# Kernel tuning notes

Measured on AMD Instinct MI355X. Metric: run time of the kernel, lower is better.

Reference implementation:

```python
import jax, jax.numpy as jnp
import numpy as np
import math

IN_CH = 256
CH = 128
SCALE = math.sqrt(CH)
TEMPERATURE = 1.0


def setup_inputs() -> dict:
    key = jax.random.key(0)
    ks = jax.random.split(key, 9)
    B, C, H, W = 8, IN_CH, 56, 56
    x = jax.random.normal(ks[0], (B, C, H, W), dtype=jnp.float32)
    s_in = 1.0 / math.sqrt(IN_CH)
    s_ch = 1.0 / math.sqrt(CH)
    wq = jax.random.uniform(ks[1], (CH, IN_CH), minval=-s_in, maxval=s_in)
    bq = jax.random.uniform(ks[2], (CH,), minval=-s_in, maxval=s_in)
    wk = jax.random.uniform(ks[3], (CH, IN_CH), minval=-s_in, maxval=s_in)
    bk = jax.random.uniform(ks[4], (CH,), minval=-s_in, maxval=s_in)
    wv = jax.random.uniform(ks[5], (CH, IN_CH), minval=-s_in, maxval=s_in)
    bv = jax.random.uniform(ks[6], (CH,), minval=-s_in, maxval=s_in)
    wo = jax.random.uniform(ks[7], (IN_CH, CH), minval=-s_ch, maxval=s_ch)
    bo = jax.random.uniform(ks[8], (IN_CH,), minval=-s_ch, maxval=s_ch)
    return {"x": x, "wq": wq, "bq": bq, "wk": wk, "bk": bk,
            "wv": wv, "bv": bv, "wo": wo, "bo": bo}


def reference(x, wq, bq, wk, bk, wv, bv, wo, bo):
    B, C, H, W = x.shape
    N = H * W
    xf = x.reshape(B, C, N)  # flatten spatial; 1x1 conv == channel matmul
    q = jnp.einsum('oc,bcn->bon', wq, xf) + bq[None, :, None]  # (B,CH,N)
    k = jnp.einsum('oc,bcn->bon', wk, xf) + bk[None, :, None]
    v = jnp.einsum('oc,bcn->bon', wv, xf) + bv[None, :, None]
    # similarity map (B, N, N): query positions x key positions
    sim = jnp.einsum('bcn,bcm->bnm', q, k) / (SCALE * TEMPERATURE)
    attn = jax.nn.softmax(sim, axis=2)
    out = jnp.einsum('bnm,bcm->bnc', attn, v)  # (B, N, CH)
    out = jnp.einsum('oc,bnc->bon', wo, out) + bo[None, :, None]  # (B,IN_CH,N)
    return x + out.reshape(B, C, H, W)
```

## Files before the change

### kernel.cpp

```cpp
#include <hip/hip_runtime.h>
#include <hip/hip_bf16.h>
#include <math.h>

#define NPOS 3136
#define NB   8
#define LOG2E 1.44269504088896f
#define QSCALE (0.08838834764831845f * LOG2E)

typedef __attribute__((ext_vector_type(8))) short shortx8;
typedef __attribute__((ext_vector_type(4))) short shortx4;
typedef __attribute__((ext_vector_type(4))) float f32x4;
typedef __attribute__((ext_vector_type(16))) float f32x16;
typedef __attribute__((ext_vector_type(4))) unsigned int uint4v;

struct S8pair { shortx4 lo, hi; };

__device__ __forceinline__ float bf2f(unsigned short u) {
    unsigned int i = ((unsigned int)u) << 16;
    return __builtin_bit_cast(float, i);
}
__device__ __forceinline__ unsigned short f2bf(float f) {
    unsigned int i = __builtin_bit_cast(unsigned int, f);
    i += 0x7FFFu + ((i >> 16) & 1u);
    return (unsigned short)(i >> 16);
}
__device__ __forceinline__ void gll16(const unsigned short* g, unsigned short* l) {
    __builtin_amdgcn_global_load_lds((const __attribute__((address_space(1))) void*)g,
                                     (__attribute__((address_space(3))) void*)l, 16, 0, 0);
}

__global__ __launch_bounds__(256) void cast_w(
    const float* __restrict__ wq, const float* __restrict__ wk,
    const float* __restrict__ wv, const float* __restrict__ wo,
    unsigned short* __restrict__ Wb)
{
    const int sel = blockIdx.y;
    const float* src = (sel == 0) ? wq : (sel == 1) ? wk : (sel == 2) ? wv : wo;
    const float sc = (sel == 0) ? QSCALE : 1.0f;
    unsigned short* dst = Wb + sel * 32768;
    int i0 = (blockIdx.x * 256 + threadIdx.x) * 8;
    #pragma unroll
    for (int e = 0; e < 8; ++e) dst[i0 + e] = f2bf(src[i0 + e] * sc);
}

__global__ __launch_bounds__(256) void cast_xT(
    const float* __restrict__ x, unsigned short* __restrict__ xT)
{
    const int b = blockIdx.z, c0 = blockIdx.y * 64, n0 = blockIdx.x * 64;
    __shared__ unsigned short Ls[64 * 66];
    const int t = threadIdx.x;
    {
        int r = t >> 2, q4 = t & 3;
        const float* src = x + ((size_t)b * 256 + c0 + r) * NPOS + n0 + q4 * 16;
        #pragma unroll
        for (int i = 0; i < 16; ++i) Ls[r * 66 + q4 * 16 + i] = f2bf(src[i]);
    }
    __syncthreads();
    {
        int j = t >> 2, h4 = t & 3;
        shortx8 v0, v1;
        #pragma unroll
        for (int i = 0; i < 8; ++i) v0[i] = (short)Ls[(h4 * 16 + i) * 66 + j];
        #pragma unroll
        for (int i = 0; i < 8; ++i) v1[i] = (short)Ls[(h4 * 16 + 8 + i) * 66 + j];
        unsigned short* dst = xT + ((size_t)b * NPOS + n0 + j) * 256 + c0 + h4 * 16;
        *reinterpret_cast<shortx8*>(dst) = v0;
        *reinterpret_cast<shortx8*>(dst + 8) = v1;
    }
}

__global__ __launch_bounds__(256) void qkv_mfma(
    const unsigned short* __restrict__ xT,
    const unsigned short* __restrict__ Wb,
    const float* __restrict__ bq, const float* __restrict__ bk, const float* __restrict__ bv,
    unsigned short* __restrict__ qT, unsigned short* __restrict__ kT,
    unsigned short* __restrict__ vC)
{
    const int b = blockIdx.z, sel = blockIdx.y, n0 = blockIdx.x * 64;
    const int t = threadIdx.x, lane = t & 63, wave = t >> 6;
    const int l16 = lane & 15, lhi = lane >> 4;
    __shared__ __align__(16) unsigned short Wt[128 * 128];
    __shared__ __align__(16) unsigned short Xt[64 * 128];
    const unsigned short* Wsel = Wb + sel * 32768;
    const float* bias = (sel == 0) ? bq : (sel == 1) ? bk : bv;

    f32x4 acc[2][4];
    #pragma unroll
    for (int ab = 0; ab < 2; ++ab)
        #pragma unroll
        for (int nb = 0; nb < 4; ++nb) acc[ab][nb] = f32x4{0.f, 0.f, 0.f, 0.f};

    for (int ks0 = 0; ks0 < 2; ++ks0) {
        const int k0 = ks0 * 128;
        __syncthreads();
        #pragma unroll
        for (int i = 0; i < 8; ++i) {
            int c = (wave * 8 + i) * 64 + lane;
            int row = c >> 4, cin = (c & 15) ^ (row & 7);
            gll16(Wsel + (size_t)row * 256 + k0 + cin * 8, &Wt[0] + (wave * 8 + i) * 512);
        }
        #pragma unroll
        for (int i = 0; i < 4; ++i) {
            int c = (wave * 4 + i) * 64 + lane;
            int row = c >> 4, cin = (c & 15) ^ (row & 7);
            gll16(xT + ((size_t)b * NPOS + n0 + row) * 256 + k0 + cin * 8,
                  &Xt[0] + (wave * 4 + i) * 512);
        }
        __syncthreads();
        #pragma unroll
        for (int ks = 0; ks < 4; ++ks) {
            shortx8 aW[2];
            #pragma unroll
            for (int ab = 0; ab < 2; ++ab) {
                int row = wave * 32 + ab * 16 + l16;
                int idx = (row * 128 + ks * 32 + lhi * 8) ^ ((row & 7) << 3);
                aW[ab] = *reinterpret_cast<const shortx8*>(Wt + idx);
            }
            #pragma unroll
            for (int nb = 0; nb < 4; ++nb) {
                int row = nb * 16 + l16;
                int idx = (row * 128 + ks * 32 + lhi * 8) ^ ((row & 7) << 3);
                shortx8 bX = *reinterpret_cast<const shortx8*>(Xt + idx);
                acc[0][nb] = __builtin_amdgcn_mfma_f32_16x16x32_bf16(aW[0], bX, acc[0][nb], 0, 0, 0);
                acc[1][nb] = __builtin_amdgcn_mfma_f32_16x16x32_bf16(aW[1], bX, acc[1][nb], 0, 0, 0);
            }
        }
    }
    const int strip = wave * 32;
    if (sel < 2) {
        unsigned short* dst0 = ((sel == 0) ? qT : kT) + (size_t)b * NPOS * 128;
        const float bsc = (sel == 0) ? QSCALE : 1.0f;
        #pragma unroll
        for (int ab = 0; ab < 2; ++ab) {
            int ocb = strip + ab * 16 + lhi * 4;
            float bb[4];
            #pragma unroll
            for (int j = 0; j < 4; ++j) bb[j] = bias[ocb + j] * bsc;
            #pragma unroll
            for (int nb = 0; nb < 4; ++nb) {
                int n = n0 + nb * 16 + l16;
                shortx4 u;
                #pragma unroll
                for (int j = 0; j < 4; ++j) u[j] = (short)f2bf(acc[ab][nb][j] + bb[j]);
                *reinterpret_cast<shortx4*>(dst0 + (size_t)n * 128 + ocb) = u;
            }
        }
    } else {
        #pragma unroll
        for (int ab = 0; ab < 2; ++ab)
            #pragma unroll
            for (int j = 0; j < 4; ++j) {
                int oc = strip + ab * 16 + lhi * 4 + j;
                float bb = bias[oc];
                unsigned short* dst = vC + ((size_t)b * 128 + oc) * NPOS + n0;
                #pragma unroll
                for (int nb = 0; nb < 4; ++nb)
                    dst[nb * 16 + l16] = f2bf(acc[ab][nb][j] + bb);
            }
    }
}

__global__ __launch_bounds__(256) void attn_kernel(
    const unsigned short* __restrict__ qT,
    const unsigned short* __restrict__ kT,
    const unsigned short* __restrict__ vC,
    unsigned short* __restrict__ ao,
    float* __restrict__ lrG)
{
    const int i_lin = blockIdx.y * 49 + blockIdx.x;
    const int b = i_lin & 7;
    const int n0 = (i_lin >> 3) * 64;
    const int t = threadIdx.x, lane = t & 63, wave = t >> 6;
    const int l31 = lane & 31, h = lane >> 5;
    const int qsub = wave >> 1, kh = wave & 1;
    const int NT = NPOS / 64;

    __shared__ __align__(16) unsigned short KsB[2][64 * 128];
    __shared__ __align__(16) unsigned short VsB[2][128 * 64];

    shortx8 aQ[8];
    {
        const unsigned short* qp = qT + ((size_t)b * NPOS + n0 + qsub * 32 + l31) * 128 + h * 8;
        #pragma unroll
        for (int kk = 0; kk < 8; ++kk)
            aQ[kk] = *reinterpret_cast<const shortx8*>(qp + kk * 16);
    }

    const unsigned short* kSrc[4];
    const unsigned short* vSrc[4];
    unsigned sDst[4];
    #pragma unroll
    for (int i = 0; i < 4; ++i) {
        int c = (wave * 4 + i) * 64 + lane;
        int rK = c >> 4, cK = (c & 15) ^ (rK & 15);
        kSrc[i] = kT + ((size_t)b * NPOS + rK) * 128 + cK * 8;
        int rV = c >> 3, cV = (c & 7) ^ (rV & 7);
        vSrc[i] = vC + ((size_t)b * 128 + rV) * NPOS + cV * 8;
        sDst[i] = (wave * 4 + i) * 512;
    }

    unsigned kIdx[8];
    {
        int rowK = kh * 32 + l31;
        #pragma unroll
        for (int kk = 0; kk < 8; ++kk)
            kIdx[kk] = rowK * 128 + (((kk * 2 + h) ^ (rowK & 15)) * 8);
    }
    unsigned vIdx[4][2][2];
    #pragma unroll
    for (int ob = 0; ob < 4; ++ob) {
        int rowV = ob * 32 + l31;
        #pragma unroll
        for (int ks = 0; ks < 2; ++ks)
            #pragma unroll
            for (int rr = 0; rr < 2; ++rr)
                vIdx[ob][ks][rr] = rowV * 64 + h * 4
                    + (((kh * 4 + ks * 2 + rr) * 8) ^ ((rowV & 7) * 8));
    }

    f32x16 o[4];
    #pragma unroll
    for (int ob = 0; ob < 4; ++ob)
        #pragma unroll
        for (int r2 = 0; r2 < 16; ++r2) o[ob][r2] = 0.f;
    float lrP = 0.f;

    f32x16 FZ;
    #pragma unroll
    for (int r2 = 0; r2 < 16; ++r2) FZ[r2] = 0.f;
    asm volatile("" : "+v"(FZ));

    #define STAGE(kt_, buf_)                                                          \
        _Pragma("unroll")                                                             \
        for (int i = 0; i < 4; ++i) {                                                 \
            gll16(kSrc[i] + (size_t)(kt_) * 8192, &KsB[buf_][0] + sDst[i]);           \
            gll16(vSrc[i] + (kt_) * 64, &VsB[buf_][0] + sDst[i]);                     \
        }

    #define COMPUTE(Ks, Vs)                                                           \
    {                                                                                 \
        f32x16 s_;                                                                    \
        __builtin_amdgcn_s_setprio(1);                                                \
        {                                                                             \
            shortx8 k0 = *reinterpret_cast<const shortx8*>((Ks) + kIdx[0]);           \
            s_ = __builtin_amdgcn_mfma_f32_32x32x16_bf16(k0, aQ[0], FZ, 0, 0, 0);     \
        }                                                                             \
        _Pragma("unroll")                                                             \
        for (int kk = 1; kk < 8; ++kk) {                                              \
            shortx8 kf = *reinterpret_cast<const shortx8*>((Ks) + kIdx[kk]);          \
            s_ = __builtin_amdgcn_mfma_f32_32x32x16_bf16(kf, aQ[kk], s_, 0, 0, 0);    \
        }                                                                             \
        __builtin_amdgcn_s_setprio(0);                                                \
        unsigned pk[8];                                                               \
        _Pragma("unroll")                                                             \
        for (int g = 0; g < 4; ++g) {                                                 \
            float p0 = exp2f(s_[g * 4 + 0]);                                          \
            float p1 = exp2f(s_[g * 4 + 1]);                                          \
            float p2 = exp2f(s_[g * 4 + 2]);                                          \
            float p3 = exp2f(s_[g * 4 + 3]);                                          \
            lrP += (p0 + p1) + (p2 + p3);                                             \
            asm("v_cvt_pk_bf16_f32 %0, %1, %2" : "=v"(pk[g * 2 + 0]) : "v"(p0), "v"(p1)); \
            asm("v_cvt_pk_bf16_f32 %0, %1, %2" : "=v"(pk[g * 2 + 1]) : "v"(p2), "v"(p3)); \
        }                                                                             \
        __builtin_amdgcn_s_setprio(1);                                                \
        _Pragma("unroll")                                                             \
        for (int ks = 0; ks < 2; ++ks) {                                              \
            uint4v pv = {pk[ks * 4 + 0], pk[ks * 4 + 1], pk[ks * 4 + 2], pk[ks * 4 + 3]}; \
            shortx8 PA = __builtin_bit_cast(shortx8, pv);                             \
            _Pragma("unroll")                                                         \
            for (int ob = 0; ob < 4; ++ob) {                                          \
                shortx4 lo = *reinterpret_cast<const shortx4*>((Vs) + vIdx[ob][ks][0]); \
                shortx4 hi = *reinterpret_cast<const shortx4*>((Vs) + vIdx[ob][ks][1]); \
                shortx8 bV = __builtin_bit_cast(shortx8, S8pair{lo, hi});             \
                o[ob] = __builtin_amdgcn_mfma_f32_32x32x16_bf16(PA, bV, o[ob], 0, 0, 0); \
            }                                                                         \
        }                                                                             \
        __builtin_amdgcn_s_setprio(0);                                                \
    }

    STAGE(0, 0)
    STAGE(1, 1)

    int cur = 0;
    for (int kt = 0; kt < NT - 1; ++kt) {
        asm volatile("s_waitcnt vmcnt(8)" ::: "memory");
        __builtin_amdgcn_sched_barrier(0);
        __builtin_amdgcn_s_barrier();
        __builtin_amdgcn_sched_barrier(0);
        COMPUTE(&KsB[cur][0], &VsB[cur][0])
        __builtin_amdgcn_sched_barrier(0);
        __builtin_amdgcn_s_barrier();
        __builtin_amdgcn_sched_barrier(0);
        if (kt < NT - 2) { STAGE(kt + 2, cur) }
        cur ^= 1;
    }
    {
        asm volatile("s_waitcnt vmcnt(0)" ::: "memory");
        __builtin_amdgcn_sched_barrier(0);
        __builtin_amdgcn_s_barrier();
        COMPUTE(&KsB[cur][0], &VsB[cur][0])
    }
    __syncthreads();

    float lr2 = lrP + __shfl_xor(lrP, 32);
    float* Om = reinterpret_cast<float*>(&KsB[0][0]);
    float* lrS = reinterpret_cast<float*>(&VsB[1][0]);
    unsigned short* Oo = &VsB[0][0];

    if (kh == 1) {
        #pragma unroll
        for (int ob = 0; ob < 4; ++ob)
            #pragma unroll
            for (int r2 = 0; r2 < 16; ++r2) {
                int q = qsub * 32 + (r2 & 3) + 8 * (r2 >> 2) + 4 * h;
                Om[q * 128 + ob * 32 + l31] = o[ob][r2];
            }
        if (lane < 32) lrS[qsub * 32 + l31] = lr2;
    }
    __syncthreads();
    if (kh == 0) {
        #pragma unroll
        for (int ob = 0; ob < 4; ++ob)
            #pragma unroll
            for (int r2 = 0; r2 < 16; ++r2) {
                int q = qsub * 32 + (r2 & 3) + 8 * (r2 >> 2) + 4 * h;
                int idx = q * 128 + ob * 32 + l31;
                Oo[idx] = f2bf(o[ob][r2] + Om[idx]);
            }
        if (lane < 32)
            lrG[(size_t)b * NPOS + n0 + qsub * 32 + l31] = lr2 + lrS[qsub * 32 + l31];
    }
    __syncthreads();
    {
        const shortx8* src = reinterpret_cast<const shortx8*>(Oo);
        shortx8* dst = reinterpret_cast<shortx8*>(ao + ((size_t)b * NPOS + n0) * 128);
        #pragma unroll
        for (int i = 0; i < 4; ++i) dst[t + 256 * i] = src[t + 256 * i];
    }
    #undef STAGE
    #undef COMPUTE
}

__global__ __launch_bounds__(256) void out_proj(
    const float* __restrict__ x,
    const unsigned short* __restrict__ Wb,
    const float* __restrict__ bo,
    const unsigned short* __restrict__ ao,
    const float* __restrict__ lrG,
    float* __restrict__ y)
{
    const int b = blockIdx.y, n0 = blockIdx.x * 64;
    const int t = threadIdx.x, lane = t & 63, wave = t >> 6;
    const int l16 = lane & 15, lhi = lane >> 4;
    __shared__ __align__(16) unsigned short Wt[256 * 128];
    __shared__ __align__(16) unsigned short At[64 * 128];
    const unsigned short* wo = Wb + 98304;

    #pragma unroll
    for (int i = 0; i < 16; ++i) {
        int c = (wave * 16 + i) * 64 + lane;
        int row = c >> 4, cin = (c & 15) ^ (row & 7);
        gll16(wo + (size_t)row * 128 + cin * 8, &Wt[0] + (wave * 16 + i) * 512);
    }
    #pragma unroll
    for (int i = 0; i < 4; ++i) {
        int c = (wave * 4 + i) * 64 + lane;
        int row = c >> 4, cin = (c & 15) ^ (row & 7);
        gll16(ao + ((size_t)b * NPOS + n0 + row) * 128 + cin * 8, &At[0] + (wave * 4 + i) * 512);
    }
    __syncthreads();

    f32x4 acc[4][4];
    #pragma unroll
    for (int ab = 0; ab < 4; ++ab)
        #pragma unroll
        for (int nb = 0; nb < 4; ++nb) acc[ab][nb] = f32x4{0.f, 0.f, 0.f, 0.f};

    const int strip = wave * 64;
    #pragma unroll
    for (int ks = 0; ks < 4; ++ks) {
        shortx8 aW[4];
        #pragma unroll
        for (int ab = 0; ab < 4; ++ab) {
            int row = strip + ab * 16 + l16;
            int idx = (row * 128 + ks * 32 + lhi * 8) ^ ((row & 7) << 3);
            aW[ab] = *reinterpret_cast<const shortx8*>(Wt + idx);
        }
        #pragma unroll
        for (int nb = 0; nb < 4; ++nb) {
            int row = nb * 16 + l16;
            int idx = (row * 128 + ks * 32 + lhi * 8) ^ ((row & 7) << 3);
            shortx8 bA = *reinterpret_cast<const shortx8*>(At + idx);
            #pragma unroll
            for (int ab = 0; ab < 4; ++ab)
                acc[ab][nb] = __builtin_amdgcn_mfma_f32_16x16x32_bf16(aW[ab], bA, acc[ab][nb], 0, 0, 0);
        }
    }

    float inv[4];
    #pragma unroll
    for (int nb = 0; nb < 4; ++nb)
        inv[nb] = 1.0f / lrG[(size_t)b * NPOS + n0 + nb * 16 + l16];

    #pragma unroll
    for (int ab = 0; ab < 4; ++ab)
        #pragma unroll
        for (int j = 0; j < 4; ++j) {
            int oc = strip + ab * 16 + lhi * 4 + j;
            float bb = bo[oc];
            const float* xr = x + ((size_t)b * 256 + oc) * NPOS + n0;
            float* yr = y + ((size_t)b * 256 + oc) * NPOS + n0;
            #pragma unroll
            for (int nb = 0; nb < 4; ++nb) {
                int n = nb * 16 + l16;
                yr[n] = xr[n] + bb + acc[ab][nb][j] * inv[nb];
            }
        }
}

extern "C" void kernel_launch(void* const* d_in, const int* in_sizes, int n_in,
                              void* d_out, int out_size, void* d_ws, size_t ws_size,
                              hipStream_t stream)
{
    const float* x  = (const float*)d_in[0];
    const float* wq = (const float*)d_in[1];
    const float* bq = (const float*)d_in[2];
    const float* wk = (const float*)d_in[3];
    const float* bk = (const float*)d_in[4];
    const float* wv = (const float*)d_in[5];
    const float* bv = (const float*)d_in[6];
    const float* wo = (const float*)d_in[7];
    const float* bo = (const float*)d_in[8];
    float* y = (float*)d_out;

    const size_t sz = (size_t)NB * NPOS * 128;
    unsigned short* qT = (unsigned short*)d_ws;
    unsigned short* kT = qT + sz;
    unsigned short* vC = kT + sz;
    unsigned short* xT = vC + sz;
    unsigned short* ao = xT;
    unsigned short* Wb = xT + 2 * sz;
    float* lrG = (float*)(Wb + 131072);

    cast_w  <<<dim3(16, 4),       256, 0, stream>>>(wq, wk, wv, wo, Wb);
    cast_xT <<<dim3(49, 4, NB),   256, 0, stream>>>(x, xT);
    qkv_mfma<<<dim3(49, 3, NB),   256, 0, stream>>>(xT, Wb, bq, bk, bv, qT, kT, vC);
    attn_kernel<<<dim3(49, NB),   256, 0, stream>>>(qT, kT, vC, ao, lrG);
    out_proj<<<dim3(49, NB),      256, 0, stream>>>(x, Wb, bo, ao, lrG, y);
}
```

Measured before the change: 115.8 us.

## Process two query tiles per attention block and software-pipeline QK, exp and PV

Each attention block now handles 128 query rows (two 64-row tiles), so every staged K/V tile is reused by both query tiles. The grid shrinks to 200 blocks, and the last tile per batch is a single-tile block. The loop is restructured so the PV MFMAs of the previous key tile run next to the QK MFMAs of the current tile, with the exp step deferred, using a triple-buffered V tile. This halves K/V global and LDS traffic per query and hides exp latency behind MFMA work. The cost is doubled accumulator register pressure (launch_bounds 256,1), fewer blocks than the 256 CUs, and redundant compute on the lone tile.

```diff
diff --git a/kernel.cpp b/kernel.cpp
--- a/kernel.cpp
+++ b/kernel.cpp
@@ -160,30 +160,34 @@
     }
 }
 
-__global__ __launch_bounds__(256) void attn_kernel(
+__global__ __launch_bounds__(256, 1) void attn_kernel(
     const unsigned short* __restrict__ qT,
     const unsigned short* __restrict__ kT,
     const unsigned short* __restrict__ vC,
     unsigned short* __restrict__ ao,
     float* __restrict__ lrG)
 {
-    const int i_lin = blockIdx.y * 49 + blockIdx.x;
-    const int b = i_lin & 7;
-    const int n0 = (i_lin >> 3) * 64;
+    const int id = blockIdx.x;
+    const int b = id & 7;
+    const int ti = id >> 3;
+    const int lone = (ti == 24);
+    const int n0 = ti * 128;
     const int t = threadIdx.x, lane = t & 63, wave = t >> 6;
     const int l31 = lane & 31, h = lane >> 5;
     const int qsub = wave >> 1, kh = wave & 1;
     const int NT = NPOS / 64;
 
     __shared__ __align__(16) unsigned short KsB[2][64 * 128];
-    __shared__ __align__(16) unsigned short VsB[2][128 * 64];
-
-    shortx8 aQ[8];
-    {
-        const unsigned short* qp = qT + ((size_t)b * NPOS + n0 + qsub * 32 + l31) * 128 + h * 8;
+    __shared__ __align__(16) unsigned short VsT[3][128 * 64];
+
+    shortx8 aQ[2][8];
+    #pragma unroll
+    for (int qt = 0; qt < 2; ++qt) {
+        int qb = n0 + (lone ? 0 : qt * 64) + qsub * 32 + l31;
+        const unsigned short* qp = qT + ((size_t)b * NPOS + qb) * 128 + h * 8;
         #pragma unroll
         for (int kk = 0; kk < 8; ++kk)
-            aQ[kk] = *reinterpret_cast<const shortx8*>(qp + kk * 16);
+            aQ[qt][kk] = *reinterpret_cast<const shortx8*>(qp + kk * 16);
     }
 
     const unsigned short* kSrc[4];
@@ -218,127 +222,164 @@
                     + (((kh * 4 + ks * 2 + rr) * 8) ^ ((rowV & 7) * 8));
     }
 
-    f32x16 o[4];
-    #pragma unroll
-    for (int ob = 0; ob < 4; ++ob)
-        #pragma unroll
-        for (int r2 = 0; r2 < 16; ++r2) o[ob][r2] = 0.f;
-    float lrP = 0.f;
+    f32x16 o[2][4];
+    #pragma unroll
+    for (int qt = 0; qt < 2; ++qt)
+        #pragma unroll
+        for (int ob = 0; ob < 4; ++ob)
+            #pragma unroll
+            for (int r2 = 0; r2 < 16; ++r2) o[qt][ob][r2] = 0.f;
+    float lrP[2] = {0.f, 0.f};
+    unsigned pkP[2][8];
 
     f32x16 FZ;
     #pragma unroll
     for (int r2 = 0; r2 < 16; ++r2) FZ[r2] = 0.f;
     asm volatile("" : "+v"(FZ));
 
-    #define STAGE(kt_, buf_)                                                          \
+    #define STAGE(kt_, kb_, vb_)                                                      \
         _Pragma("unroll")                                                             \
         for (int i = 0; i < 4; ++i) {                                                 \
-            gll16(kSrc[i] + (size_t)(kt_) * 8192, &KsB[buf_][0] + sDst[i]);           \
-            gll16(vSrc[i] + (kt_) * 64, &VsB[buf_][0] + sDst[i]);                     \
-        }
-
-    #define COMPUTE(Ks, Vs)                                                           \
-    {                                                                                 \
-        f32x16 s_;                                                                    \
-        __builtin_amdgcn_s_setprio(1);                                                \
+            gll16(kSrc[i] + (size_t)(kt_) * 8192, &KsB[kb_][0] + sDst[i]);            \
+            gll16(vSrc[i] + (kt_) * 64, &VsT[vb_][0] + sDst[i]);                      \
+        }
+
+    #define QK2(Ks)                                                                   \
         {                                                                             \
-            shortx8 k0 = *reinterpret_cast<const shortx8*>((Ks) + kIdx[0]);           \
-            s_ = __builtin_amdgcn_mfma_f32_32x32x16_bf16(k0, aQ[0], FZ, 0, 0, 0);     \
-        }                                                                             \
-        _Pragma("unroll")                                                             \
-        for (int kk = 1; kk < 8; ++kk) {                                              \
-            shortx8 kf = *reinterpret_cast<const shortx8*>((Ks) + kIdx[kk]);          \
-            s_ = __builtin_amdgcn_mfma_f32_32x32x16_bf16(kf, aQ[kk], s_, 0, 0, 0);    \
-        }                                                                             \
-        __builtin_amdgcn_s_setprio(0);                                                \
-        unsigned pk[8];                                                               \
-        _Pragma("unroll")                                                             \
-        for (int g = 0; g < 4; ++g) {                                                 \
-            float p0 = exp2f(s_[g * 4 + 0]);                                          \
-            float p1 = exp2f(s_[g * 4 + 1]);                                          \
-            float p2 = exp2f(s_[g * 4 + 2]);                                          \
-            float p3 = exp2f(s_[g * 4 + 3]);                                          \
-            lrP += (p0 + p1) + (p2 + p3);                                             \
-            asm("v_cvt_pk_bf16_f32 %0, %1, %2" : "=v"(pk[g * 2 + 0]) : "v"(p0), "v"(p1)); \
-            asm("v_cvt_pk_bf16_f32 %0, %1, %2" : "=v"(pk[g * 2 + 1]) : "v"(p2), "v"(p3)); \
-        }                                                                             \
-        __builtin_amdgcn_s_setprio(1);                                                \
+            shortx8 kf0 = *reinterpret_cast<const shortx8*>((Ks) + kIdx[0]);          \
+            s0_ = __builtin_amdgcn_mfma_f32_32x32x16_bf16(kf0, aQ[0][0], FZ, 0, 0, 0);\
+            s1_ = __builtin_amdgcn_mfma_f32_32x32x16_bf16(kf0, aQ[1][0], FZ, 0, 0, 0);\
+            _Pragma("unroll")                                                         \
+            for (int kk = 1; kk < 8; ++kk) {                                          \
+                shortx8 kf = *reinterpret_cast<const shortx8*>((Ks) + kIdx[kk]);      \
+                s0_ = __builtin_amdgcn_mfma_f32_32x32x16_bf16(kf, aQ[0][kk], s0_, 0, 0, 0); \
+                s1_ = __builtin_amdgcn_mfma_f32_32x32x16_bf16(kf, aQ[1][kk], s1_, 0, 0, 0); \
+            }                                                                         \
+        }
+
+    #define PV2(Vs)                                                                   \
         _Pragma("unroll")                                                             \
         for (int ks = 0; ks < 2; ++ks) {                                              \
-            uint4v pv = {pk[ks * 4 + 0], pk[ks * 4 + 1], pk[ks * 4 + 2], pk[ks * 4 + 3]}; \
-            shortx8 PA = __builtin_bit_cast(shortx8, pv);                             \
+            uint4v pv0 = {pkP[0][ks * 4 + 0], pkP[0][ks * 4 + 1],                     \
+                          pkP[0][ks * 4 + 2], pkP[0][ks * 4 + 3]};                    \
+            uint4v pv1 = {pkP[1][ks * 4 + 0], pkP[1][ks * 4 + 1],                     \
+                          pkP[1][ks * 4 + 2], pkP[1][ks * 4 + 3]};                    \
+            shortx8 PA0 = __builtin_bit_cast(shortx8, pv0);                           \
+            shortx8 PA1 = __builtin_bit_cast(shortx8, pv1);                           \
             _Pragma("unroll")                                                         \
             for (int ob = 0; ob < 4; ++ob) {                                          \
                 shortx4 lo = *reinterpret_cast<const shortx4*>((Vs) + vIdx[ob][ks][0]); \
                 shortx4 hi = *reinterpret_cast<const shortx4*>((Vs) + vIdx[ob][ks][1]); \
                 shortx8 bV = __builtin_bit_cast(shortx8, S8pair{lo, hi});             \
-                o[ob] = __builtin_amdgcn_mfma_f32_32x32x16_bf16(PA, bV, o[ob], 0, 0, 0); \
+                o[0][ob] = __builtin_amdgcn_mfma_f32_32x32x16_bf16(PA0, bV, o[0][ob], 0, 0, 0); \
+                o[1][ob] = __builtin_amdgcn_mfma_f32_32x32x16_bf16(PA1, bV, o[1][ob], 0, 0, 0); \
             }                                                                         \
-        }                                                                             \
-        __builtin_amdgcn_s_setprio(0);                                                \
-    }
-
-    STAGE(0, 0)
-    STAGE(1, 1)
-
-    int cur = 0;
-    for (int kt = 0; kt < NT - 1; ++kt) {
+        }
+
+    #define EXP_ONE(S, QT)                                                            \
+        _Pragma("unroll")                                                             \
+        for (int g = 0; g < 4; ++g) {                                                 \
+            float p0 = exp2f((S)[g * 4 + 0]);                                         \
+            float p1 = exp2f((S)[g * 4 + 1]);                                         \
+            float p2 = exp2f((S)[g * 4 + 2]);                                         \
+            float p3 = exp2f((S)[g * 4 + 3]);                                         \
+            lrP[QT] += (p0 + p1) + (p2 + p3);                                         \
+            asm("v_cvt_pk_bf16_f32 %0, %1, %2" : "=v"(pkP[QT][g * 2 + 0]) : "v"(p0), "v"(p1)); \
+            asm("v_cvt_pk_bf16_f32 %0, %1, %2" : "=v"(pkP[QT][g * 2 + 1]) : "v"(p2), "v"(p3)); \
+        }
+
+    #define SB __builtin_amdgcn_sched_barrier(0)
+
+    STAGE(0, 0, 0)
+    STAGE(1, 1, 1)
+
+    {
         asm volatile("s_waitcnt vmcnt(8)" ::: "memory");
-        __builtin_amdgcn_sched_barrier(0);
-        __builtin_amdgcn_s_barrier();
-        __builtin_amdgcn_sched_barrier(0);
-        COMPUTE(&KsB[cur][0], &VsB[cur][0])
-        __builtin_amdgcn_sched_barrier(0);
-        __builtin_amdgcn_s_barrier();
-        __builtin_amdgcn_sched_barrier(0);
-        if (kt < NT - 2) { STAGE(kt + 2, cur) }
-        cur ^= 1;
-    }
+        SB; __builtin_amdgcn_s_barrier(); SB;
+        f32x16 s0_, s1_;
+        __builtin_amdgcn_s_setprio(1);
+        QK2(&KsB[0][0])
+        __builtin_amdgcn_s_setprio(0);
+        EXP_ONE(s0_, 0) EXP_ONE(s1_, 1)
+        SB; __builtin_amdgcn_s_barrier(); SB;
+        STAGE(2, 0, 2)
+    }
+
+    int vp = 0;
+    for (int kt = 1; kt <= NT - 2; ++kt) {
+        asm volatile("s_waitcnt vmcnt(8)" ::: "memory");
+        SB; __builtin_amdgcn_s_barrier(); SB;
+        f32x16 s0_, s1_;
+        __builtin_amdgcn_s_setprio(1);
+        QK2(&KsB[kt & 1][0])
+        PV2(&VsT[vp][0])
+        __builtin_amdgcn_s_setprio(0);
+        EXP_ONE(s0_, 0) EXP_ONE(s1_, 1)
+        SB; __builtin_amdgcn_s_barrier(); SB;
+        if (kt <= NT - 3) { STAGE(kt + 2, kt & 1, vp) }
+        vp = (vp == 2) ? 0 : vp + 1;
+    }
+
     {
         asm volatile("s_waitcnt vmcnt(0)" ::: "memory");
-        __builtin_amdgcn_sched_barrier(0);
-        __builtin_amdgcn_s_barrier();
-        COMPUTE(&KsB[cur][0], &VsB[cur][0])
+        SB; __builtin_amdgcn_s_barrier(); SB;
+        f32x16 s0_, s1_;
+        __builtin_amdgcn_s_setprio(1);
+        QK2(&KsB[0][0])
+        PV2(&VsT[2][0])
+        __builtin_amdgcn_s_setprio(0);
+        EXP_ONE(s0_, 0) EXP_ONE(s1_, 1)
+        __builtin_amdgcn_s_setprio(1);
+        PV2(&VsT[0][0])
+        __builtin_amdgcn_s_setprio(0);
     }
     __syncthreads();
 
-    float lr2 = lrP + __shfl_xor(lrP, 32);
     float* Om = reinterpret_cast<float*>(&KsB[0][0]);
-    float* lrS = reinterpret_cast<float*>(&VsB[1][0]);
-    unsigned short* Oo = &VsB[0][0];
-
-    if (kh == 1) {
-        #pragma unroll
-        for (int ob = 0; ob < 4; ++ob)
-            #pragma unroll
-            for (int r2 = 0; r2 < 16; ++r2) {
-                int q = qsub * 32 + (r2 & 3) + 8 * (r2 >> 2) + 4 * h;
-                Om[q * 128 + ob * 32 + l31] = o[ob][r2];
-            }
-        if (lane < 32) lrS[qsub * 32 + l31] = lr2;
-    }
-    __syncthreads();
-    if (kh == 0) {
-        #pragma unroll
-        for (int ob = 0; ob < 4; ++ob)
-            #pragma unroll
-            for (int r2 = 0; r2 < 16; ++r2) {
-                int q = qsub * 32 + (r2 & 3) + 8 * (r2 >> 2) + 4 * h;
-                int idx = q * 128 + ob * 32 + l31;
-                Oo[idx] = f2bf(o[ob][r2] + Om[idx]);
-            }
-        if (lane < 32)
-            lrG[(size_t)b * NPOS + n0 + qsub * 32 + l31] = lr2 + lrS[qsub * 32 + l31];
-    }
-    __syncthreads();
-    {
-        const shortx8* src = reinterpret_cast<const shortx8*>(Oo);
-        shortx8* dst = reinterpret_cast<shortx8*>(ao + ((size_t)b * NPOS + n0) * 128);
-        #pragma unroll
-        for (int i = 0; i < 4; ++i) dst[t + 256 * i] = src[t + 256 * i];
+    float* lrS = reinterpret_cast<float*>(&VsT[1][0]);
+    unsigned short* Oo = &VsT[0][0];
+
+    for (int qt = 0; qt < (lone ? 1 : 2); ++qt) {
+        float lr2 = lrP[qt] + __shfl_xor(lrP[qt], 32);
+        if (kh == 1) {
+            #pragma unroll
+            for (int ob = 0; ob < 4; ++ob)
+                #pragma unroll
+                for (int r2 = 0; r2 < 16; ++r2) {
+                    int q = qsub * 32 + (r2 & 3) + 8 * (r2 >> 2) + 4 * h;
+                    Om[q * 128 + ob * 32 + l31] = o[qt][ob][r2];
+                }
+            if (lane < 32) lrS[qsub * 32 + l31] = lr2;
+        }
+        __syncthreads();
+        if (kh == 0) {
+            #pragma unroll
+            for (int ob = 0; ob < 4; ++ob)
+                #pragma unroll
+                for (int r2 = 0; r2 < 16; ++r2) {
+                    int q = qsub * 32 + (r2 & 3) + 8 * (r2 >> 2) + 4 * h;
+                    int idx = q * 128 + ob * 32 + l31;
+                    Oo[idx] = f2bf(o[qt][ob][r2] + Om[idx]);
+                }
+            if (lane < 32)
+                lrG[(size_t)b * NPOS + n0 + qt * 64 + qsub * 32 + l31]
+                    = lr2 + lrS[qsub * 32 + l31];
+        }
+        __syncthreads();
+        {
+            const shortx8* src = reinterpret_cast<const shortx8*>(Oo);
+            shortx8* dst = reinterpret_cast<shortx8*>(
+                ao + ((size_t)b * NPOS + n0 + qt * 64) * 128);
+            #pragma unroll
+            for (int i = 0; i < 4; ++i) dst[t + 256 * i] = src[t + 256 * i];
+        }
+        __syncthreads();
     }
     #undef STAGE
-    #undef COMPUTE
+    #undef QK2
+    #undef PV2
+    #undef EXP_ONE
+    #undef SB
 }
 
 __global__ __launch_bounds__(256) void out_proj(
@@ -445,6 +486,6 @@
     cast_w  <<<dim3(16, 4),       256, 0, stream>>>(wq, wk, wv, wo, Wb);
     cast_xT <<<dim3(49, 4, NB),   256, 0, stream>>>(x, xT);
     qkv_mfma<<<dim3(49, 3, NB),   256, 0, stream>>>(xT, Wb, bq, bk, bv, qT, kT, vC);
-    attn_kernel<<<dim3(49, NB),   256, 0, stream>>>(qT, kT, vC, ao, lrG);
+    attn_kernel<<<dim3(200),      256, 0, stream>>>(qT, kT, vC, ao, lrG);
     out_proj<<<dim3(49, NB),      256, 0, stream>>>(x, Wb, bo, ao, lrG, y);
 }
```

Measured after the change: 133.7 us. +15.5%, slower.

## Fuse x transpose-cast into QKV projection and triple-buffer attention K/V staging

Applied to the files above, without the earlier changes.

Removes the separate cast_xT kernel: each QKV block now converts and transposes its x tile into a swizzled LDS buffer once and reuses it for all three projections, avoiding the bf16 xT round trip through global memory and a launch. The cost is that the QKV grid shrinks from 1176 to 392 blocks with larger LDS use, which lowers parallelism and occupancy. In the attention kernel, K/V staging moves from double to triple buffering so the next-next tile load is issued before compute with one barrier per iteration instead of two. This raises LDS per block to about 96KB and may reduce blocks per CU.

```diff
diff --git a/kernel.cpp b/kernel.cpp
--- a/kernel.cpp
+++ b/kernel.cpp
@@ -43,120 +43,115 @@
     for (int e = 0; e < 8; ++e) dst[i0 + e] = f2bf(src[i0 + e] * sc);
 }
 
-__global__ __launch_bounds__(256) void cast_xT(
-    const float* __restrict__ x, unsigned short* __restrict__ xT)
-{
-    const int b = blockIdx.z, c0 = blockIdx.y * 64, n0 = blockIdx.x * 64;
-    __shared__ unsigned short Ls[64 * 66];
-    const int t = threadIdx.x;
-    {
-        int r = t >> 2, q4 = t & 3;
-        const float* src = x + ((size_t)b * 256 + c0 + r) * NPOS + n0 + q4 * 16;
-        #pragma unroll
-        for (int i = 0; i < 16; ++i) Ls[r * 66 + q4 * 16 + i] = f2bf(src[i]);
-    }
-    __syncthreads();
-    {
-        int j = t >> 2, h4 = t & 3;
-        shortx8 v0, v1;
-        #pragma unroll
-        for (int i = 0; i < 8; ++i) v0[i] = (short)Ls[(h4 * 16 + i) * 66 + j];
-        #pragma unroll
-        for (int i = 0; i < 8; ++i) v1[i] = (short)Ls[(h4 * 16 + 8 + i) * 66 + j];
-        unsigned short* dst = xT + ((size_t)b * NPOS + n0 + j) * 256 + c0 + h4 * 16;
-        *reinterpret_cast<shortx8*>(dst) = v0;
-        *reinterpret_cast<shortx8*>(dst + 8) = v1;
-    }
-}
-
-__global__ __launch_bounds__(256) void qkv_mfma(
-    const unsigned short* __restrict__ xT,
+__global__ __launch_bounds__(256) void qkv_fused(
+    const float* __restrict__ x,
     const unsigned short* __restrict__ Wb,
     const float* __restrict__ bq, const float* __restrict__ bk, const float* __restrict__ bv,
     unsigned short* __restrict__ qT, unsigned short* __restrict__ kT,
     unsigned short* __restrict__ vC)
 {
-    const int b = blockIdx.z, sel = blockIdx.y, n0 = blockIdx.x * 64;
+    const int b = blockIdx.y, n0 = blockIdx.x * 64;
     const int t = threadIdx.x, lane = t & 63, wave = t >> 6;
     const int l16 = lane & 15, lhi = lane >> 4;
+    __shared__ __align__(16) unsigned short Xt[64 * 256];
     __shared__ __align__(16) unsigned short Wt[128 * 128];
-    __shared__ __align__(16) unsigned short Xt[64 * 128];
-    const unsigned short* Wsel = Wb + sel * 32768;
-    const float* bias = (sel == 0) ? bq : (sel == 1) ? bk : bv;
-
-    f32x4 acc[2][4];
-    #pragma unroll
-    for (int ab = 0; ab < 2; ++ab)
-        #pragma unroll
-        for (int nb = 0; nb < 4; ++nb) acc[ab][nb] = f32x4{0.f, 0.f, 0.f, 0.f};
-
-    for (int ks0 = 0; ks0 < 2; ++ks0) {
-        const int k0 = ks0 * 128;
+    __shared__ unsigned short Ls[64 * 66];
+
+    for (int cc = 0; cc < 4; ++cc) {
+        {
+            int r = t >> 2, q4 = t & 3;
+            const float* src = x + ((size_t)b * 256 + cc * 64 + r) * NPOS + n0 + q4 * 16;
+            #pragma unroll
+            for (int i = 0; i < 16; ++i) Ls[r * 66 + q4 * 16 + i] = f2bf(src[i]);
+        }
         __syncthreads();
-        #pragma unroll
-        for (int i = 0; i < 8; ++i) {
-            int c = (wave * 8 + i) * 64 + lane;
-            int row = c >> 4, cin = (c & 15) ^ (row & 7);
-            gll16(Wsel + (size_t)row * 256 + k0 + cin * 8, &Wt[0] + (wave * 8 + i) * 512);
-        }
-        #pragma unroll
-        for (int i = 0; i < 4; ++i) {
-            int c = (wave * 4 + i) * 64 + lane;
-            int row = c >> 4, cin = (c & 15) ^ (row & 7);
-            gll16(xT + ((size_t)b * NPOS + n0 + row) * 256 + k0 + cin * 8,
-                  &Xt[0] + (wave * 4 + i) * 512);
+        {
+            int j = t >> 2, h4 = t & 3;
+            shortx8 v0, v1;
+            #pragma unroll
+            for (int i = 0; i < 8; ++i) v0[i] = (short)Ls[(h4 * 16 + i) * 66 + j];
+            #pragma unroll
+            for (int i = 0; i < 8; ++i) v1[i] = (short)Ls[(h4 * 16 + 8 + i) * 66 + j];
+            int X = (j & 7) << 3;
+            int c0 = cc * 64 + h4 * 16;
+            *reinterpret_cast<shortx8*>(&Xt[j * 256 + (c0 ^ X)]) = v0;
+            *reinterpret_cast<shortx8*>(&Xt[j * 256 + ((c0 + 8) ^ X)]) = v1;
         }
         __syncthreads();
-        #pragma unroll
-        for (int ks = 0; ks < 4; ++ks) {
-            shortx8 aW[2];
+    }
+
+    for (int sel = 0; sel < 3; ++sel) {
+        const unsigned short* Wsel = Wb + sel * 32768;
+        const float* bias = (sel == 0) ? bq : (sel == 1) ? bk : bv;
+
+        f32x4 acc[2][4];
+        #pragma unroll
+        for (int ab = 0; ab < 2; ++ab)
+            #pragma unroll
+            for (int nb = 0; nb < 4; ++nb) acc[ab][nb] = f32x4{0.f, 0.f, 0.f, 0.f};
+
+        for (int ks0 = 0; ks0 < 2; ++ks0) {
+            const int k0 = ks0 * 128;
+            __syncthreads();
+            #pragma unroll
+            for (int i = 0; i < 8; ++i) {
+                int c = (wave * 8 + i) * 64 + lane;
+                int row = c >> 4, cin = (c & 15) ^ (row & 7);
+                gll16(Wsel + (size_t)row * 256 + k0 + cin * 8, &Wt[0] + (wave * 8 + i) * 512);
+            }
+            __syncthreads();
+            #pragma unroll
+            for (int ks = 0; ks < 4; ++ks) {
+                shortx8 aW[2];
+                #pragma unroll
+                for (int ab = 0; ab < 2; ++ab) {
+                    int row = wave * 32 + ab * 16 + l16;
+                    int idx = (row * 128 + ks * 32 + lhi * 8) ^ ((row & 7) << 3);
+                    aW[ab] = *reinterpret_cast<const shortx8*>(Wt + idx);
+                }
+                #pragma unroll
+                for (int nb = 0; nb < 4; ++nb) {
+                    int row = nb * 16 + l16;
+                    int idx = row * 256 + ((k0 + ks * 32 + lhi * 8) ^ ((row & 7) << 3));
+                    shortx8 bX = *reinterpret_cast<const shortx8*>(Xt + idx);
+                    acc[0][nb] = __builtin_amdgcn_mfma_f32_16x16x32_bf16(aW[0], bX, acc[0][nb], 0, 0, 0);
+                    acc[1][nb] = __builtin_amdgcn_mfma_f32_16x16x32_bf16(aW[1], bX, acc[1][nb], 0, 0, 0);
+                }
+            }
+        }
+
+        const int strip = wave * 32;
+        if (sel < 2) {
+            unsigned short* dst0 = ((sel == 0) ? qT : kT) + (size_t)b * NPOS * 128;
+            const float bsc = (sel == 0) ? QSCALE : 1.0f;
             #pragma unroll
             for (int ab = 0; ab < 2; ++ab) {
-                int row = wave * 32 + ab * 16 + l16;
-                int idx = (row * 128 + ks * 32 + lhi * 8) ^ ((row & 7) << 3);
-                aW[ab] = *reinterpret_cast<const shortx8*>(Wt + idx);
-            }
-            #pragma unroll
-            for (int nb = 0; nb < 4; ++nb) {
-                int row = nb * 16 + l16;
-                int idx = (row * 128 + ks * 32 + lhi * 8) ^ ((row & 7) << 3);
-                shortx8 bX = *reinterpret_cast<const shortx8*>(Xt + idx);
-                acc[0][nb] = __builtin_amdgcn_mfma_f32_16x16x32_bf16(aW[0], bX, acc[0][nb], 0, 0, 0);
-                acc[1][nb] = __builtin_amdgcn_mfma_f32_16x16x32_bf16(aW[1], bX, acc[1][nb], 0, 0, 0);
-            }
-        }
-    }
-    const int strip = wave * 32;
-    if (sel < 2) {
-        unsigned short* dst0 = ((sel == 0) ? qT : kT) + (size_t)b * NPOS * 128;
-        const float bsc = (sel == 0) ? QSCALE : 1.0f;
-        #pragma unroll
-        for (int ab = 0; ab < 2; ++ab) {
-            int ocb = strip + ab * 16 + lhi * 4;
-            float bb[4];
-            #pragma unroll
-            for (int j = 0; j < 4; ++j) bb[j] = bias[ocb + j] * bsc;
-            #pragma unroll
-            for (int nb = 0; nb < 4; ++nb) {
-                int n = n0 + nb * 16 + l16;
-                shortx4 u;
+                int ocb = strip + ab * 16 + lhi * 4;
+                float bb[4];
                 #pragma unroll
-                for (int j = 0; j < 4; ++j) u[j] = (short)f2bf(acc[ab][nb][j] + bb[j]);
-                *reinterpret_cast<shortx4*>(dst0 + (size_t)n * 128 + ocb) = u;
-            }
-        }
-    } else {
-        #pragma unroll
-        for (int ab = 0; ab < 2; ++ab)
-            #pragma unroll
-            for (int j = 0; j < 4; ++j) {
-                int oc = strip + ab * 16 + lhi * 4 + j;
-                float bb = bias[oc];
-                unsigned short* dst = vC + ((size_t)b * 128 + oc) * NPOS + n0;
+                for (int j = 0; j < 4; ++j) bb[j] = bias[ocb + j] * bsc;
                 #pragma unroll
-                for (int nb = 0; nb < 4; ++nb)
-                    dst[nb * 16 + l16] = f2bf(acc[ab][nb][j] + bb);
-            }
+                for (int nb = 0; nb < 4; ++nb) {
+                    int n = n0 + nb * 16 + l16;
+                    shortx4 u;
+                    #pragma unroll
+                    for (int j = 0; j < 4; ++j) u[j] = (short)f2bf(acc[ab][nb][j] + bb[j]);
+                    *reinterpret_cast<shortx4*>(dst0 + (size_t)n * 128 + ocb) = u;
+                }
+            }
+        } else {
+            #pragma unroll
+            for (int ab = 0; ab < 2; ++ab)
+                #pragma unroll
+                for (int j = 0; j < 4; ++j) {
+                    int oc = strip + ab * 16 + lhi * 4 + j;
+                    float bb = bias[oc];
+                    unsigned short* dst = vC + ((size_t)b * 128 + oc) * NPOS + n0;
+                    #pragma unroll
+                    for (int nb = 0; nb < 4; ++nb)
+                        dst[nb * 16 + l16] = f2bf(acc[ab][nb][j] + bb);
+                }
+        }
     }
 }
 
@@ -175,8 +170,9 @@
     const int qsub = wave >> 1, kh = wave & 1;
     const int NT = NPOS / 64;
 
-    __shared__ __align__(16) unsigned short KsB[2][64 * 128];
-    __shared__ __align__(16) unsigned short VsB[2][128 * 64];
+    __shared__ __align__(16) unsigned short KsB[3][64 * 128];
+    __shared__ __align__(16) unsigned short VsB[3][128 * 64];
+    __shared__ float lrS[64];
 
     shortx8 aQ[8];
     {
@@ -278,33 +274,29 @@
         __builtin_amdgcn_s_setprio(0);                                                \
     }
 
+    #define SB __builtin_amdgcn_sched_barrier(0)
+
     STAGE(0, 0)
     STAGE(1, 1)
 
-    int cur = 0;
+    int rd = 0, wr = 2;
     for (int kt = 0; kt < NT - 1; ++kt) {
         asm volatile("s_waitcnt vmcnt(8)" ::: "memory");
-        __builtin_amdgcn_sched_barrier(0);
-        __builtin_amdgcn_s_barrier();
-        __builtin_amdgcn_sched_barrier(0);
-        COMPUTE(&KsB[cur][0], &VsB[cur][0])
-        __builtin_amdgcn_sched_barrier(0);
-        __builtin_amdgcn_s_barrier();
-        __builtin_amdgcn_sched_barrier(0);
-        if (kt < NT - 2) { STAGE(kt + 2, cur) }
-        cur ^= 1;
+        SB; __builtin_amdgcn_s_barrier(); SB;
+        if (kt < NT - 2) { STAGE(kt + 2, wr) }
+        COMPUTE(&KsB[rd][0], &VsB[rd][0])
+        rd = (rd == 2) ? 0 : rd + 1;
+        wr = (wr == 2) ? 0 : wr + 1;
     }
     {
         asm volatile("s_waitcnt vmcnt(0)" ::: "memory");
-        __builtin_amdgcn_sched_barrier(0);
-        __builtin_amdgcn_s_barrier();
-        COMPUTE(&KsB[cur][0], &VsB[cur][0])
+        SB; __builtin_amdgcn_s_barrier(); SB;
+        COMPUTE(&KsB[rd][0], &VsB[rd][0])
     }
     __syncthreads();
 
     float lr2 = lrP + __shfl_xor(lrP, 32);
     float* Om = reinterpret_cast<float*>(&KsB[0][0]);
-    float* lrS = reinterpret_cast<float*>(&VsB[1][0]);
     unsigned short* Oo = &VsB[0][0];
 
     if (kh == 1) {
@@ -339,6 +331,7 @@
     }
     #undef STAGE
     #undef COMPUTE
+    #undef SB
 }
 
 __global__ __launch_bounds__(256) void out_proj(
@@ -437,14 +430,12 @@
     unsigned short* qT = (unsigned short*)d_ws;
     unsigned short* kT = qT + sz;
     unsigned short* vC = kT + sz;
-    unsigned short* xT = vC + sz;
-    unsigned short* ao = xT;
-    unsigned short* Wb = xT + 2 * sz;
+    unsigned short* ao = vC + sz;
+    unsigned short* Wb = ao + sz;
     float* lrG = (float*)(Wb + 131072);
 
-    cast_w  <<<dim3(16, 4),       256, 0, stream>>>(wq, wk, wv, wo, Wb);
-    cast_xT <<<dim3(49, 4, NB),   256, 0, stream>>>(x, xT);
-    qkv_mfma<<<dim3(49, 3, NB),   256, 0, stream>>>(xT, Wb, bq, bk, bv, qT, kT, vC);
-    attn_kernel<<<dim3(49, NB),   256, 0, stream>>>(qT, kT, vC, ao, lrG);
-    out_proj<<<dim3(49, NB),      256, 0, stream>>>(x, Wb, bo, ao, lrG, y);
-}
+    cast_w   <<<dim3(16, 4),     256, 0, stream>>>(wq, wk, wv, wo, Wb);
+    qkv_fused<<<dim3(49, NB),    256, 0, stream>>>(x, Wb, bq, bk, bv, qT, kT, vC);
+    attn_kernel<<<dim3(49, NB),  256, 0, stream>>>(qT, kT, vC, ao, lrG);
+    out_proj <<<dim3(49, NB),    256, 0, stream>>>(x, Wb, bo, ao, lrG, y);
+}
```

Result: slower. 170.8 us (+47.4%).
